# Kernel optimization log

Measured on AMD Instinct MI355X. Metric: run time of the kernel, lower is better.

The kernel has to match this reference:

```python
import jax, jax.numpy as jnp
import numpy as np

B, C, H, W = 4, 256, 128, 128
K = 3
BN = max(16, C // 4)  # 64
PAD = K // 2
EPS = 1e-5


def conv2d(x, w, b=None, pad=0):
    out = jax.lax.conv_general_dilated(
        x, w, (1, 1), [(pad, pad), (pad, pad)],
        dimension_numbers=("NCHW", "OIHW", "NCHW"))
    if b is not None:
        out = out + b[None, :, None, None]
    return out


def deform_conv2d(z, offset, mask, w, b):
    # torchvision modulated deform conv v2: offset [B,2*K*K,H,W] interleaved (dy,dx),
    # mask [B,K*K,H,W], kernel positions row-major, stride 1, pad PAD.
    Bz, Cb, Hz, Wz = z.shape
    K2 = K * K
    off = offset.reshape(Bz, K2, 2, Hz, Wz)
    ky, kx = jnp.meshgrid(jnp.arange(K), jnp.arange(K), indexing="ij")
    # sampling positions py/px: [B, K2, H, W]
    py = off[:, :, 0] + jnp.arange(Hz)[None, None, :, None] + (ky.reshape(K2) - PAD)[None, :, None, None]
    px = off[:, :, 1] + jnp.arange(Wz)[None, None, None, :] + (kx.reshape(K2) - PAD)[None, :, None, None]
    y0 = jnp.floor(py)
    x0 = jnp.floor(px)
    wy1 = py - y0  # frac weights
    wx1 = px - x0
    z_flat = z.reshape(Bz, Cb, Hz * Wz)

    def gather(yy, xx, wgt):
        valid = (yy >= 0) & (yy < Hz) & (xx >= 0) & (xx < Wz)
        yc = jnp.clip(yy, 0, Hz - 1).astype(jnp.int32)
        xc = jnp.clip(xx, 0, Wz - 1).astype(jnp.int32)
        idx = (yc * Wz + xc).reshape(Bz, K2 * Hz * Wz)
        g = jnp.take_along_axis(z_flat, idx[:, None, :], axis=2)  # [B, Cb, K2*H*W]
        g = g.reshape(Bz, Cb, K2, Hz, Wz)
        return g * (wgt * valid.astype(z.dtype))[:, None]

    val = (gather(y0, x0, (1 - wy1) * (1 - wx1))
           + gather(y0, x0 + 1, (1 - wy1) * wx1)
           + gather(y0 + 1, x0, wy1 * (1 - wx1))
           + gather(y0 + 1, x0 + 1, wy1 * wx1))
    val = val * mask[:, None]  # modulate: [B, Cb, K2, H, W]
    out = jnp.einsum("bckhw,ock->bohw", val, w.reshape(w.shape[0], Cb, K2))
    return out + b[None, :, None, None]


def setup_inputs() -> dict:
    key = jax.random.key(0)
    ks = jax.random.split(key, 11)
    s = 0.05
    return {
        "x": jax.random.normal(ks[0], (B, C, H, W), jnp.float32),
        "down_w": jax.random.normal(ks[1], (BN, C, 1, 1), jnp.float32) * s,
        "off_w": jax.random.normal(ks[2], (2 * K * K, BN, 3, 3), jnp.float32) * s,
        "off_b": jax.random.normal(ks[3], (2 * K * K,), jnp.float32) * s,
        "mask_w": jax.random.normal(ks[4], (K * K, BN, 3, 3), jnp.float32) * s,
        "mask_b": jax.random.normal(ks[5], (K * K,), jnp.float32) * s,
        "def_w": jax.random.normal(ks[6], (BN, BN, K, K), jnp.float32) * s,
        "def_b": jax.random.normal(ks[7], (BN,), jnp.float32) * s,
        "up_w": jax.random.normal(ks[8], (C, BN, 1, 1), jnp.float32) * s,
        "gamma": jnp.ones((C,), jnp.float32),
        "beta": jnp.zeros((C,), jnp.float32),
    }


def reference(x, down_w, off_w, off_b, mask_w, mask_b, def_w, def_b, up_w, gamma, beta):
    z = conv2d(x, down_w)                               # 1x1 down: [B, BN, H, W]
    offset = conv2d(z, off_w, off_b, pad=1)             # [B, 18, H, W]
    mask = jax.nn.sigmoid(conv2d(z, mask_w, mask_b, pad=1))  # [B, 9, H, W]
    z = deform_conv2d(z, offset, mask, def_w, def_b)    # [B, BN, H, W]
    z = conv2d(z, up_w)                                 # 1x1 up: [B, C, H, W]
    y = x + z
    # BatchNorm2d in training mode: batch statistics over (B, H, W), biased var
    mean = jnp.mean(y, axis=(0, 2, 3), keepdims=True)
    var = jnp.var(y, axis=(0, 2, 3), keepdims=True)
    yh = (y - mean) * jax.lax.rsqrt(var + EPS)
    yh = yh * gamma[None, :, None, None] + beta[None, :, None, None]
    return yh * jax.nn.sigmoid(yh)  # SiLU
```

## Files before the change

kernel.cpp:

```cpp
#include <hip/hip_runtime.h>
#include <hip/hip_bf16.h>


typedef __attribute__((ext_vector_type(8))) short bf16x8;
typedef __attribute__((ext_vector_type(4))) float f32x4;

#define HW   16384
#define CC   256
#define BNC  64

#define WS_STATS   0
#define WS_SS      131072
#define WS_FD      135168
#define WS_FOM     167936
#define WS_FDEF    204800
#define WS_FUP     278528
#define WS_ZBF     311296
#define WS_OM      8699904
#define WS_Z2      15777792

__device__ __forceinline__ short f2b(float f) {
    unsigned u = __float_as_uint(f);
    unsigned r = (u + 0x7FFFu + ((u >> 16) & 1u)) >> 16;
    return (short)r;
}
__device__ __forceinline__ float b2f(short s) {
    return __uint_as_float(((unsigned)(unsigned short)s) << 16);
}

__global__ void k_prep(const float* __restrict__ down_w, const float* __restrict__ off_w,
                       const float* __restrict__ mask_w, const float* __restrict__ def_w,
                       const float* __restrict__ up_w, char* __restrict__ ws) {
    int g = blockIdx.x * 256 + threadIdx.x;
    int row = g >> 6, lane = g & 63;
    if (row >= 172) return;
    int l15 = lane & 15, q = lane >> 4;
    short vals[8];
    short* dst;
    if (row < 32) {
        int nt = row >> 3, kk = row & 7;
        int n = nt * 16 + l15;
        for (int j = 0; j < 8; ++j) {
            int c = kk * 32 + q * 8 + j;
            vals[j] = f2b(down_w[n * 256 + c]);
        }
        dst = (short*)(ws + WS_FD) + row * 512 + lane * 8;
    } else if (row < 68) {
        int r = row - 32; int nt = r / 18, kk = r % 18;
        int n = nt * 16 + l15;
        for (int j = 0; j < 8; ++j) {
            int kap = kk * 32 + q * 8 + j; int k = kap >> 6, c = kap & 63;
            float v = 0.f;
            if (n < 18)      v = off_w[(n * 64 + c) * 9 + k];
            else if (n < 27) v = mask_w[((n - 18) * 64 + c) * 9 + k];
            vals[j] = f2b(v);
        }
        dst = (short*)(ws + WS_FOM) + r * 512 + lane * 8;
    } else if (row < 140) {
        int r = row - 68; int nt = r / 18, kk = r % 18;
        int n = nt * 16 + l15;
        int u = kk * 4 + q, k = u >> 3;
        for (int j = 0; j < 8; ++j) {
            int c = (u & 7) * 8 + j;
            vals[j] = f2b(def_w[(n * 64 + c) * 9 + k]);
        }
        dst = (short*)(ws + WS_FDEF) + r * 512 + lane * 8;
    } else {
        int r = row - 140; int nt = r >> 1, kk = r & 1;
        int o = nt * 16 + l15;
        for (int j = 0; j < 8; ++j) {
            int c = kk * 32 + q * 8 + j;
            vals[j] = f2b(up_w[o * 64 + c]);
        }
        dst = (short*)(ws + WS_FUP) + r * 512 + lane * 8;
    }
    for (int j = 0; j < 8; ++j) dst[j] = vals[j];
}

__global__ __launch_bounds__(256) void k_down(const float* __restrict__ x,
                                              const short* __restrict__ wfd,
                                              short* __restrict__ zbf) {
    __shared__ __align__(16) short xl[64 * 264];
    int blk = blockIdx.x;
    int b = blk >> 8;
    int hw0 = (blk & 255) * 64;
    int t = threadIdx.x;
    const float* xb = x + (size_t)b * CC * HW + hw0;
    int px = t & 63, w = t >> 6;
    for (int h = 0; h < 8; ++h) {
        int c0 = h * 32 + w * 8;
        bf16x8 pk;
        #pragma unroll
        for (int j = 0; j < 8; ++j)
            pk[j] = f2b(xb[(size_t)(c0 + j) * HW + px]);
        *(bf16x8*)(&xl[px * 264 + c0]) = pk;
    }
    __syncthreads();
    int lane = t & 63, wv = t >> 6;
    int l15 = lane & 15, q = lane >> 4;
    bf16x8 A[8];
    const short* xrow = &xl[(wv * 16 + l15) * 264];
    for (int kk = 0; kk < 8; ++kk)
        A[kk] = *(const bf16x8*)(xrow + kk * 32 + q * 8);
    const bf16x8* Bp = (const bf16x8*)wfd;
    size_t obase = ((size_t)b * HW + hw0 + wv * 16) * 64;
    for (int nt = 0; nt < 4; ++nt) {
        f32x4 acc = {0.f, 0.f, 0.f, 0.f};
        for (int kk = 0; kk < 8; ++kk) {
            bf16x8 Bf = Bp[(nt * 8 + kk) * 64 + lane];
            acc = __builtin_amdgcn_mfma_f32_16x16x32_bf16(A[kk], Bf, acc, 0, 0, 0);
        }
        int n = nt * 16 + l15;
        for (int r = 0; r < 4; ++r) {
            int prow = q * 4 + r;
            zbf[obase + (size_t)prow * 64 + n] = f2b(acc[r]);
        }
    }
}

__global__ __launch_bounds__(256) void k_offmask(const short* __restrict__ zbf,
                                                 const short* __restrict__ wfom,
                                                 const float* __restrict__ off_b,
                                                 const float* __restrict__ mask_b,
                                                 float* __restrict__ om) {
    int blk = blockIdx.x;
    int b = blk >> 8;
    int hw0 = (blk & 255) * 64;
    int y = hw0 >> 7, x0 = hw0 & 127;
    int t = threadIdx.x, lane = t & 63, wv = t >> 6;
    int l15 = lane & 15, q = lane >> 4;
    int xx0 = x0 + wv * 16 + l15;
    const short* zb = zbf + (size_t)b * HW * 64;
    f32x4 acc0 = {0, 0, 0, 0}, acc1 = {0, 0, 0, 0};
    const bf16x8* Bp = (const bf16x8*)wfom;
    for (int kk = 0; kk < 18; ++kk) {
        int k = kk >> 1;
        int yy = y + (k / 3) - 1;
        int xx = xx0 + (k % 3) - 1;
        int c0 = (kk & 1) * 32 + q * 8;
        bf16x8 A = {0, 0, 0, 0, 0, 0, 0, 0};
        if (yy >= 0 && yy < 128 && xx >= 0 && xx < 128)
            A = *(const bf16x8*)(zb + ((size_t)(yy * 128 + xx)) * 64 + c0);
        bf16x8 B0 = Bp[kk * 64 + lane];
        bf16x8 B1 = Bp[(18 + kk) * 64 + lane];
        acc0 = __builtin_amdgcn_mfma_f32_16x16x32_bf16(A, B0, acc0, 0, 0, 0);
        acc1 = __builtin_amdgcn_mfma_f32_16x16x32_bf16(A, B1, acc1, 0, 0, 0);
    }
    float* omb = om + ((size_t)b * HW + hw0 + wv * 16) * 27;
    for (int half = 0; half < 2; ++half) {
        f32x4 acc = half ? acc1 : acc0;
        int n = half * 16 + l15;
        if (n < 27) {
            for (int r = 0; r < 4; ++r) {
                int prow = q * 4 + r;
                float v = acc[r];
                if (n < 18) v += off_b[n];
                else { v += mask_b[n - 18]; v = 1.f / (1.f + __expf(-v)); }
                omb[prow * 27 + n] = v;
            }
        }
    }
}

__global__ __launch_bounds__(256) void k_deform(const short* __restrict__ zbf,
                                                const float* __restrict__ om,
                                                const short* __restrict__ wfdef,
                                                const float* __restrict__ def_b,
                                                short* __restrict__ z2) {
    __shared__ int4   pAi4[144];
    __shared__ float4 pAw4[144];
    __shared__ __align__(16) short valA[18 * 64 * 8];
    int blk = blockIdx.x;
    int b = blk >> 10;
    int hw0 = (blk & 1023) * 16;
    int y = hw0 >> 7, x0 = hw0 & 127;
    int t = threadIdx.x;
    if (t < 144) {
        int px = t / 9, k = t % 9;
        const float* p = om + ((size_t)b * HW + hw0 + px) * 27;
        float dy = p[2 * k], dx = p[2 * k + 1], m = p[18 + k];
        float py  = (float)y + (float)(k / 3 - 1) + dy;
        float pxf = (float)(x0 + px) + (float)(k % 3 - 1) + dx;
        float fy = floorf(py), fx = floorf(pxf);
        int iy = (int)fy, ix = (int)fx;
        float wy = py - fy, wx = pxf - fx;
        float ww[4] = { (1.f - wy) * (1.f - wx) * m, (1.f - wy) * wx * m,
                        wy * (1.f - wx) * m,          wy * wx * m };
        int ys[2] = {iy, iy + 1}, xs[2] = {ix, ix + 1};
        int   ri[4]; float rw[4];
        for (int ci = 0; ci < 4; ++ci) {
            int cy = ys[ci >> 1], cx = xs[ci & 1];
            bool v = (cy >= 0 && cy < 128 && cx >= 0 && cx < 128);
            ri[ci] = v ? (cy * 128 + cx) * 64 : 0;
            rw[ci] = v ? ww[ci] : 0.f;
        }
        pAi4[t] = make_int4(ri[0], ri[1], ri[2], ri[3]);
        pAw4[t] = make_float4(rw[0], rw[1], rw[2], rw[3]);
    }
    __syncthreads();
    const unsigned short* zb = (const unsigned short*)zbf + (size_t)b * HW * 64;
    for (int s = t; s < 1152; s += 256) {
        int px = s & 15, u = s >> 4;
        int k = u >> 3, cg = u & 7;
        int task = px * 9 + k;
        int4   idx = pAi4[task];
        float4 wt  = pAw4[task];
        int   ii[4] = { idx.x, idx.y, idx.z, idx.w };
        float wwt[4] = { wt.x, wt.y, wt.z, wt.w };
        float acc[8] = {0.f, 0.f, 0.f, 0.f, 0.f, 0.f, 0.f, 0.f};
        #pragma unroll
        for (int ci = 0; ci < 4; ++ci) {
            float w = wwt[ci];
            int4 d = *(const int4*)(zb + ii[ci] + cg * 8);
            int dp[4] = { d.x, d.y, d.z, d.w };
            #pragma unroll
            for (int p = 0; p < 4; ++p) {
                float lo = __uint_as_float((unsigned)dp[p] << 16);
                float hi = __uint_as_float((unsigned)dp[p] & 0xffff0000u);
                acc[2 * p]     += w * lo;
                acc[2 * p + 1] += w * hi;
            }
        }
        bf16x8 out;
        #pragma unroll
        for (int j = 0; j < 8; ++j) out[j] = f2b(acc[j]);
        *(bf16x8*)(&valA[s * 8]) = out;
    }
    __syncthreads();
    int lane = t & 63, wv = t >> 6;
    int l15 = lane & 15, q = lane >> 4;
    f32x4 acc = {0, 0, 0, 0};
    const bf16x8* Bp = (const bf16x8*)wfdef;
    const bf16x8* Ap = (const bf16x8*)valA;
    for (int kk = 0; kk < 18; ++kk) {
        bf16x8 A  = Ap[kk * 64 + lane];
        bf16x8 Bf = Bp[(wv * 18 + kk) * 64 + lane];
        acc = __builtin_amdgcn_mfma_f32_16x16x32_bf16(A, Bf, acc, 0, 0, 0);
    }
    int n = wv * 16 + l15;
    float bias = def_b[n];
    short* z2b = z2 + ((size_t)b * HW + hw0) * 64;
    for (int r = 0; r < 4; ++r) {
        int prow = q * 4 + r;
        z2b[prow * 64 + n] = f2b(acc[r] + bias);
    }
}

__global__ __launch_bounds__(256) void k_up(const short* __restrict__ z2,
                                            const short* __restrict__ wfup,
                                            const float* __restrict__ x,
                                            float* __restrict__ yout,
                                            float* __restrict__ stats) {
    __shared__ float yl[16 * 257];
    int blk = blockIdx.x;
    int b = blk >> 10;
    int hw0 = (blk & 1023) * 16;
    int t = threadIdx.x, lane = t & 63, wv = t >> 6;
    int l15 = lane & 15, q = lane >> 4;
    const short* z2b = z2 + ((size_t)b * HW + hw0) * 64;
    bf16x8 A0 = *(const bf16x8*)(z2b + (size_t)l15 * 64 + q * 8);
    bf16x8 A1 = *(const bf16x8*)(z2b + (size_t)l15 * 64 + 32 + q * 8);
    const bf16x8* Bp = (const bf16x8*)wfup;
    for (int ntl = 0; ntl < 4; ++ntl) {
        int nt = wv * 4 + ntl;
        f32x4 acc = {0, 0, 0, 0};
        acc = __builtin_amdgcn_mfma_f32_16x16x32_bf16(A0, Bp[(nt * 2 + 0) * 64 + lane], acc, 0, 0, 0);
        acc = __builtin_amdgcn_mfma_f32_16x16x32_bf16(A1, Bp[(nt * 2 + 1) * 64 + lane], acc, 0, 0, 0);
        int o = nt * 16 + l15;
        for (int r = 0; r < 4; ++r) yl[(q * 4 + r) * 257 + o] = acc[r];
    }
    __syncthreads();
    int o = t;
    size_t pbase = (size_t)b * CC * HW + (size_t)o * HW + hw0;
    const float4* xv = (const float4*)(x + pbase);
    float4* yv = (float4*)(yout + pbase);
    float s = 0.f, s2 = 0.f;
    #pragma unroll
    for (int g4 = 0; g4 < 4; ++g4) {
        float4 xvv = xv[g4];
        float xf[4] = { xvv.x, xvv.y, xvv.z, xvv.w };
        float of[4];
        #pragma unroll
        for (int j = 0; j < 4; ++j) {
            int px = g4 * 4 + j;
            float v = yl[px * 257 + o] + xf[j];
            of[j] = v;
            s += v; s2 += v * v;
        }
        yv[g4] = make_float4(of[0], of[1], of[2], of[3]);
    }
    int bucket = blk & 63;
    atomicAdd(&stats[bucket * 512 + o], s);
    atomicAdd(&stats[bucket * 512 + 256 + o], s2);
}

__global__ void k_stats(const float* __restrict__ stats, const float* __restrict__ gamma,
                        const float* __restrict__ beta, float* __restrict__ ss) {
    int o = threadIdx.x;
    float s = 0.f, s2 = 0.f;
    for (int u = 0; u < 64; ++u) { s += stats[u * 512 + o]; s2 += stats[u * 512 + 256 + o]; }
    float mean = s * (1.f / 65536.f);
    float var  = s2 * (1.f / 65536.f) - mean * mean;
    float rs = rsqrtf(var + 1e-5f);
    float sc = gamma[o] * rs;
    ss[o]       = sc;
    ss[256 + o] = beta[o] - mean * sc;
}

__global__ __launch_bounds__(256) void k_bn(float* __restrict__ y, const float* __restrict__ ss) {
    int g = blockIdx.x * 256 + threadIdx.x;
    int o = (g >> 10) & 255;
    float sc = ss[o], sh = ss[256 + o];
    float4* p = (float4*)y + (size_t)g * 4;
    for (int i = 0; i < 4; ++i) {
        float4 v = p[i];
        float vf[4] = { v.x, v.y, v.z, v.w };
        for (int j = 0; j < 4; ++j) {
            float h = vf[j] * sc + sh;
            vf[j] = h / (1.f + __expf(-h));
        }
        p[i] = make_float4(vf[0], vf[1], vf[2], vf[3]);
    }
}

extern "C" void kernel_launch(void* const* d_in, const int* in_sizes, int n_in,
                              void* d_out, int out_size, void* d_ws, size_t ws_size,
                              hipStream_t stream) {
    const float* x      = (const float*)d_in[0];
    const float* down_w = (const float*)d_in[1];
    const float* off_w  = (const float*)d_in[2];
    const float* off_b  = (const float*)d_in[3];
    const float* mask_w = (const float*)d_in[4];
    const float* mask_b = (const float*)d_in[5];
    const float* def_w  = (const float*)d_in[6];
    const float* def_b  = (const float*)d_in[7];
    const float* up_w   = (const float*)d_in[8];
    const float* gamma  = (const float*)d_in[9];
    const float* beta   = (const float*)d_in[10];
    char* ws = (char*)d_ws;
    float* stats = (float*)(ws + WS_STATS);
    float* ss    = (float*)(ws + WS_SS);
    short* wfd   = (short*)(ws + WS_FD);
    short* wfom  = (short*)(ws + WS_FOM);
    short* wfdef = (short*)(ws + WS_FDEF);
    short* wfup  = (short*)(ws + WS_FUP);
    short* zbf   = (short*)(ws + WS_ZBF);
    float* om    = (float*)(ws + WS_OM);
    short* z2    = (short*)(ws + WS_Z2);
    float* y     = (float*)d_out;

    hipMemsetAsync(stats, 0, 64 * 512 * sizeof(float), stream);
    hipLaunchKernelGGL(k_prep,    dim3(43),   dim3(256), 0, stream, down_w, off_w, mask_w, def_w, up_w, ws);
    hipLaunchKernelGGL(k_down,    dim3(1024), dim3(256), 0, stream, x, wfd, zbf);
    hipLaunchKernelGGL(k_offmask, dim3(1024), dim3(256), 0, stream, zbf, wfom, off_b, mask_b, om);
    hipLaunchKernelGGL(k_deform,  dim3(4096), dim3(256), 0, stream, zbf, om, wfdef, def_b, z2);
    hipLaunchKernelGGL(k_up,      dim3(4096), dim3(256), 0, stream, z2, wfup, x, y, stats);
    hipLaunchKernelGGL(k_stats,   dim3(1),    dim3(256), 0, stream, stats, gamma, beta, ss);
    hipLaunchKernelGGL(k_bn,      dim3(4096), dim3(256), 0, stream, y, ss);
}
```

Baseline: 271.9 us.

## Widen k_up tiles to 64 pixels with coalesced row access and shuffle reductions

k_up now handles 64 pixels per block instead of 16, with each wave computing its own 16-pixel slice across all 256 output channels. The up-projection results are staged in LDS as bf16, transposed to channel-major with padding. The epilogue assigns 16 threads per channel row, so each float4 read of x and write of y covers 256 contiguous bytes rather than a short 64-byte strip per thread. Partial statistics are combined with wave shuffles before the atomics, which reduces atomic count. The risks are an extra bf16 rounding on the up-conv output before the residual add, and a grid shrunk to 1024 blocks.

```diff
diff --git a/kernel.cpp b/kernel.cpp
--- a/kernel.cpp
+++ b/kernel.cpp
@@ -3,6 +3,7 @@
 
 
 typedef __attribute__((ext_vector_type(8))) short bf16x8;
+typedef __attribute__((ext_vector_type(4))) short bf16x4;
 typedef __attribute__((ext_vector_type(4))) float f32x4;
 
 #define HW   16384
@@ -251,47 +252,50 @@
                                             const float* __restrict__ x,
                                             float* __restrict__ yout,
                                             float* __restrict__ stats) {
-    __shared__ float yl[16 * 257];
+    __shared__ __align__(16) short yl[256 * 70];
     int blk = blockIdx.x;
-    int b = blk >> 10;
-    int hw0 = (blk & 1023) * 16;
+    int b = blk >> 8;
+    int hw0 = (blk & 255) * 64;
     int t = threadIdx.x, lane = t & 63, wv = t >> 6;
     int l15 = lane & 15, q = lane >> 4;
-    const short* z2b = z2 + ((size_t)b * HW + hw0) * 64;
+    const short* z2b = z2 + ((size_t)b * HW + hw0 + wv * 16) * 64;
     bf16x8 A0 = *(const bf16x8*)(z2b + (size_t)l15 * 64 + q * 8);
     bf16x8 A1 = *(const bf16x8*)(z2b + (size_t)l15 * 64 + 32 + q * 8);
     const bf16x8* Bp = (const bf16x8*)wfup;
-    for (int ntl = 0; ntl < 4; ++ntl) {
-        int nt = wv * 4 + ntl;
+    for (int nt = 0; nt < 16; ++nt) {
         f32x4 acc = {0, 0, 0, 0};
         acc = __builtin_amdgcn_mfma_f32_16x16x32_bf16(A0, Bp[(nt * 2 + 0) * 64 + lane], acc, 0, 0, 0);
         acc = __builtin_amdgcn_mfma_f32_16x16x32_bf16(A1, Bp[(nt * 2 + 1) * 64 + lane], acc, 0, 0, 0);
         int o = nt * 16 + l15;
-        for (int r = 0; r < 4; ++r) yl[(q * 4 + r) * 257 + o] = acc[r];
+        bf16x4 pk;
+        #pragma unroll
+        for (int r = 0; r < 4; ++r) pk[r] = f2b(acc[r]);
+        *(bf16x4*)(&yl[o * 70 + wv * 16 + q * 4]) = pk;
     }
     __syncthreads();
-    int o = t;
-    size_t pbase = (size_t)b * CC * HW + (size_t)o * HW + hw0;
-    const float4* xv = (const float4*)(x + pbase);
-    float4* yv = (float4*)(yout + pbase);
-    float s = 0.f, s2 = 0.f;
+    int i16 = t & 15, og = t >> 4;
+    int bucket = blk & 63;
+    size_t base = (size_t)b * CC * HW + hw0 + (size_t)i16 * 4;
     #pragma unroll
-    for (int g4 = 0; g4 < 4; ++g4) {
-        float4 xvv = xv[g4];
-        float xf[4] = { xvv.x, xvv.y, xvv.z, xvv.w };
-        float of[4];
-        #pragma unroll
-        for (int j = 0; j < 4; ++j) {
-            int px = g4 * 4 + j;
-            float v = yl[px * 257 + o] + xf[j];
-            of[j] = v;
-            s += v; s2 += v * v;
-        }
-        yv[g4] = make_float4(of[0], of[1], of[2], of[3]);
-    }
-    int bucket = blk & 63;
-    atomicAdd(&stats[bucket * 512 + o], s);
-    atomicAdd(&stats[bucket * 512 + 256 + o], s2);
+    for (int i = 0; i < 16; ++i) {
+        int o = og + 16 * i;
+        size_t pb = base + (size_t)o * HW;
+        float4 xv = *(const float4*)(x + pb);
+        bf16x4 uv = *(const bf16x4*)(&yl[o * 70 + i16 * 4]);
+        float v0 = b2f(uv[0]) + xv.x;
+        float v1 = b2f(uv[1]) + xv.y;
+        float v2 = b2f(uv[2]) + xv.z;
+        float v3 = b2f(uv[3]) + xv.w;
+        *(float4*)(yout + pb) = make_float4(v0, v1, v2, v3);
+        float s  = v0 + v1 + v2 + v3;
+        float s2 = v0 * v0 + v1 * v1 + v2 * v2 + v3 * v3;
+        #pragma unroll
+        for (int m = 8; m >= 1; m >>= 1) { s += __shfl_xor(s, m); s2 += __shfl_xor(s2, m); }
+        if (i16 == 0) {
+            atomicAdd(&stats[bucket * 512 + o], s);
+            atomicAdd(&stats[bucket * 512 + 256 + o], s2);
+        }
+    }
 }
 
 __global__ void k_stats(const float* __restrict__ stats, const float* __restrict__ gamma,
@@ -354,7 +358,7 @@
     hipLaunchKernelGGL(k_down,    dim3(1024), dim3(256), 0, stream, x, wfd, zbf);
     hipLaunchKernelGGL(k_offmask, dim3(1024), dim3(256), 0, stream, zbf, wfom, off_b, mask_b, om);
     hipLaunchKernelGGL(k_deform,  dim3(4096), dim3(256), 0, stream, zbf, om, wfdef, def_b, z2);
-    hipLaunchKernelGGL(k_up,      dim3(4096), dim3(256), 0, stream, z2, wfup, x, y, stats);
+    hipLaunchKernelGGL(k_up,      dim3(1024), dim3(256), 0, stream, z2, wfup, x, y, stats);
     hipLaunchKernelGGL(k_stats,   dim3(1),    dim3(256), 0, stream, stats, gamma, beta, ss);
     hipLaunchKernelGGL(k_bn,      dim3(4096), dim3(256), 0, stream, y, ss);
 }
```

New measurement: 251.2 us. 1.08x faster.
